# Optimization experiments

Measured on AMD Instinct MI355X. Metric: run time of the kernel, lower is better.

## Reference

```python
import jax, jax.numpy as jnp
import numpy as np

B, L, D, H = 8, 2048, 1024, 1024
BASE_LR, BASE_WD = 0.01, 0.9


def setup_inputs() -> dict:
    key = jax.random.key(0)
    ks = jax.random.split(key, 8)
    s = 1.0 / np.sqrt(D)
    return {
        "x": jax.random.normal(ks[0], (B, L, D), jnp.float32),
        "hidden": jax.random.normal(ks[1], (B, D, H), jnp.float32),
        "log_base_lr": jnp.array([np.log(BASE_LR)], jnp.float32),
        "w_lr": jax.random.normal(ks[2], (D, 1), jnp.float32) * s,
        "b_lr": jnp.zeros((1,), jnp.float32),
        "log_base_wd": jnp.array([np.log(BASE_WD)], jnp.float32),
        "w_wd": jax.random.normal(ks[3], (D, 1), jnp.float32) * s,
        "b_wd": jnp.zeros((1,), jnp.float32),
        "w_q": jax.random.normal(ks[4], (D, H), jnp.float32) * s,
        "b_q": jnp.zeros((H,), jnp.float32),
        "w_k": jax.random.normal(ks[5], (D, H), jnp.float32) * s,
        "b_k": jnp.zeros((H,), jnp.float32),
        "w_v": jax.random.normal(ks[6], (D, D), jnp.float32) * s,
        "b_v": jnp.zeros((D,), jnp.float32),
    }


def reference(x, hidden, log_base_lr, w_lr, b_lr, log_base_wd, w_wd, b_wd,
              w_q, b_q, w_k, b_k, w_v, b_v):
    batch, length, dim = x.shape
    W_prev = hidden  # [b, d, h]
    query = x @ w_q + b_q                     # [b, l, h]
    key = x @ w_k + b_k                       # [b, l, h]
    value = x @ w_v + b_v                     # [b, l, d]
    lr = jnp.exp(log_base_lr) * jax.nn.sigmoid((x @ w_lr + b_lr)[..., 0])  # [b, l]
    # log(1 - base_wd * sigmoid(.)) via log1p for stability; same math.
    log_wd = jnp.log1p(-jnp.exp(log_base_wd) * jax.nn.sigmoid((x @ w_wd + b_wd)[..., 0]))  # [b, l]
    wd_cross = jnp.exp(jnp.cumsum(log_wd, axis=1))  # [b, l]
    # inner-chunk decay: entry [b, m, l] = exp(sum_{j=m+1..l} log_wd[b, j]) for l >= m
    tri = jnp.triu(jnp.broadcast_to(log_wd[:, None, :], (batch, length, length)), k=1)
    wd_inner = jnp.triu(jnp.exp(jnp.cumsum(tri, axis=2)))  # [b, l, l]
    kq = jnp.einsum('bld,bmd->blm', key, query)            # [b, l, m]
    mask_kq = kq * wd_inner
    WpK_V = jnp.einsum('bdh,blh->bld', W_prev, key) - value  # [b, l, d]
    y_inner = -jnp.einsum('bld,bl,blm->bmd', WpK_V, lr, mask_kq)
    y_cross = jnp.einsum('bdh,blh,bl->bld', W_prev, query, wd_cross)
    y = y_inner + y_cross
    W_next_inner = -jnp.einsum('bld,bl,blh->bdh', WpK_V, lr * wd_inner[:, :, -1], key)
    W_next_cross = W_prev * wd_cross[:, -1][:, None, None]
    W_next = W_next_inner + W_next_cross
    return y, W_next
```

## Files before the change

### kernel.cpp

```cpp
#include <hip/hip_runtime.h>
#include <stdint.h>

#define BB 8
#define LL 2048
#define DD 1024
#define HH 1024
#define BL (BB*LL)

typedef __attribute__((ext_vector_type(8))) short short8;
typedef __attribute__((ext_vector_type(4))) float f32x4;

__device__ __forceinline__ unsigned short f2bf(float f) {
  unsigned int x = __float_as_uint(f);
  unsigned int r = (x + 0x7fffu + ((x >> 16) & 1u)) >> 16;
  return (unsigned short)r;
}
__device__ __forceinline__ float bf2f(unsigned short u) {
  return __uint_as_float(((unsigned int)u) << 16);
}

__device__ __forceinline__ void stage16(const unsigned short* g, unsigned short* l) {
  __builtin_amdgcn_global_load_lds((const __attribute__((address_space(1))) void*)g,
                                   (__attribute__((address_space(3))) void*)l,
                                   16, 0, 0);
}

#define TM 128
#define TN 128
#define BK 64

struct __align__(16) Smem {
  unsigned short a[TM*BK];
  unsigned short b[TN*BK];
};

__device__ __forceinline__ void gemm_core(const unsigned short* __restrict__ A, int lda,
                                          const unsigned short* __restrict__ B, int ldb,
                                          int m0, int n0, int ktiles,
                                          Smem* sm, f32x4 acc[4][4]) {
  const int tid  = threadIdx.x;
  const int lane = tid & 63;
  const int wave = tid >> 6;
  const int mw = (wave >> 1) * 64;
  const int nw = (wave & 1) * 64;
  const int srow = lane >> 3;
  const int scol = (((lane & 7) ^ srow) * 8);
  const int fk = (lane >> 4) * 8;
  const int fr = lane & 15;
  const int fx = fr & 7;
  for (int kt = 0; kt < ktiles; ++kt) {
    const int k0 = kt * BK;
#pragma unroll
    for (int r = 0; r < 4; ++r) {
      const int chunk = wave * 4 + r;
      const int row = chunk * 8 + srow;
      stage16(A + (size_t)(m0 + row) * lda + (k0 + scol), &sm->a[chunk * 512]);
      stage16(B + (size_t)(n0 + row) * ldb + (k0 + scol), &sm->b[chunk * 512]);
    }
    __syncthreads();
#pragma unroll
    for (int kk = 0; kk < BK; kk += 32) {
      const int kc = ((((kk + fk) >> 3) ^ fx) << 3);
      short8 af[4], bfv[4];
#pragma unroll
      for (int i = 0; i < 4; ++i)
        af[i] = *(const short8*)&sm->a[(mw + i*16 + fr) * BK + kc];
#pragma unroll
      for (int j = 0; j < 4; ++j)
        bfv[j] = *(const short8*)&sm->b[(nw + j*16 + fr) * BK + kc];
#pragma unroll
      for (int i = 0; i < 4; ++i)
#pragma unroll
        for (int j = 0; j < 4; ++j)
          acc[i][j] = __builtin_amdgcn_mfma_f32_16x16x32_bf16(af[i], bfv[j], acc[i][j], 0, 0, 0);
    }
    __syncthreads();
  }
}

__device__ __forceinline__ void acc_init(f32x4 acc[4][4]) {
#pragma unroll
  for (int i = 0; i < 4; ++i)
#pragma unroll
    for (int j = 0; j < 4; ++j)
      acc[i][j] = (f32x4){0.f, 0.f, 0.f, 0.f};
}

template <typename F>
__device__ __forceinline__ void epilogue_loop(const f32x4 acc[4][4], F body) {
  const int lane_ = threadIdx.x & 63;
  const int wave_ = threadIdx.x >> 6;
  const int mw_ = (wave_ >> 1) * 64, nw_ = (wave_ & 1) * 64;
#pragma unroll
  for (int mi = 0; mi < 4; ++mi)
#pragma unroll
    for (int ni = 0; ni < 4; ++ni)
#pragma unroll
      for (int j = 0; j < 4; ++j) {
        const int rr = mw_ + mi * 16 + ((lane_ >> 4) << 2) + j;
        const int cc = nw_ + ni * 16 + (lane_ & 15);
        body(rr, cc, acc[mi][ni][j]);
      }
}

template<int MI>
struct __align__(16) Smem2 {
  unsigned short a[2][MI*2048];
  unsigned short b[2][16384];
};

template<int MI>
__device__ __forceinline__ void acc_init2(f32x4 (&acc)[MI][4]) {
#pragma unroll
  for (int i = 0; i < MI; ++i)
#pragma unroll
    for (int j = 0; j < 4; ++j)
      acc[i][j] = (f32x4){0.f, 0.f, 0.f, 0.f};
}

template<int MI, class FA, class FB>
__device__ __forceinline__ void gemm2_core(FA srcA, FB srcB, int NK,
                                           Smem2<MI>* sm, f32x4 (&acc)[MI][4]) {
  const int lane = threadIdx.x & 63;
  const int wave = threadIdx.x >> 6;
  const int srow = lane >> 3;
  const int scol = ((lane & 7) ^ srow) * 8;
  constexpr int APW = MI / 2;
  const int fk = (lane >> 4) * 8;
  const int fr = lane & 15;
  const int fx = fr & 7;
  const int mwr = (wave >> 2) * (MI * 16);
  const int nwr = (wave & 3) * 64;

  auto STAGE = [&](int p, int kt) {
#pragma unroll
    for (int r = 0; r < APW; ++r) {
      const int chunk = wave * APW + r;
      stage16(srcA(chunk * 8 + srow, kt) + scol, &sm->a[p][chunk * 512]);
    }
#pragma unroll
    for (int r = 0; r < 4; ++r) {
      const int chunk = wave * 4 + r;
      stage16(srcB(chunk * 8 + srow, kt) + scol, &sm->b[p][chunk * 512]);
    }
  };
  auto COMPUTE = [&](int p) {
    const unsigned short* pa  = sm->a[p];
    const unsigned short* pbp = sm->b[p];
#pragma unroll
    for (int kk = 0; kk < 64; kk += 32) {
      const int kc = ((((kk + fk) >> 3) ^ fx) << 3);
      short8 af[MI], bfv[4];
#pragma unroll
      for (int i = 0; i < MI; ++i)
        af[i] = *(const short8*)&pa[(mwr + i*16 + fr) * 64 + kc];
#pragma unroll
      for (int j = 0; j < 4; ++j)
        bfv[j] = *(const short8*)&pbp[(nwr + j*16 + fr) * 64 + kc];
#pragma unroll
      for (int i = 0; i < MI; ++i)
#pragma unroll
        for (int j = 0; j < 4; ++j)
          acc[i][j] = __builtin_amdgcn_mfma_f32_16x16x32_bf16(af[i], bfv[j], acc[i][j], 0, 0, 0);
    }
  };

  STAGE(0, 0);
  asm volatile("s_waitcnt vmcnt(0)" ::: "memory");
  __builtin_amdgcn_s_barrier();
  __builtin_amdgcn_sched_barrier(0);
  int cur = 0;
  for (int kt = 0; kt < NK - 1; ++kt) {
    STAGE(cur ^ 1, kt + 1);
    COMPUTE(cur);
    asm volatile("s_waitcnt vmcnt(0)" ::: "memory");
    __builtin_amdgcn_s_barrier();
    __builtin_amdgcn_sched_barrier(0);
    cur ^= 1;
  }
  COMPUTE(cur);
}

template<int MI, typename F>
__device__ __forceinline__ void epi2(const f32x4 (&acc)[MI][4], F body) {
  const int lane = threadIdx.x & 63;
  const int wave = threadIdx.x >> 6;
  const int mwr = (wave >> 2) * (MI * 16), nwr = (wave & 3) * 64;
#pragma unroll
  for (int i = 0; i < MI; ++i)
#pragma unroll
    for (int j = 0; j < 4; ++j)
#pragma unroll
      for (int jj = 0; jj < 4; ++jj) {
        const int rr = mwr + i * 16 + ((lane >> 4) << 2) + jj;
        const int cc = nwr + j * 16 + (lane & 15);
        body(rr, cc, acc[i][j][jj]);
      }
}


__global__ void k_prep_x(const float* __restrict__ x, const float* __restrict__ wlr,
                         const float* __restrict__ wwd, unsigned short* __restrict__ xb,
                         float* __restrict__ lrlog, float* __restrict__ wdlog) {
  const int wave = threadIdx.x >> 6, lane = threadIdx.x & 63;
  const int row = blockIdx.x * 4 + wave;
  const float* xr = x + (size_t)row * DD;
  float s1 = 0.f, s2 = 0.f;
#pragma unroll
  for (int ch = 0; ch < 4; ++ch) {
    const int col = ch * 256 + lane * 4;
    float4 v = *(const float4*)(xr + col);
    float4 a = *(const float4*)(wlr + col);
    float4 b = *(const float4*)(wwd + col);
    s1 += v.x*a.x + v.y*a.y + v.z*a.z + v.w*a.w;
    s2 += v.x*b.x + v.y*b.y + v.z*b.z + v.w*b.w;
    uint2 u;
    u.x = (unsigned)f2bf(v.x) | ((unsigned)f2bf(v.y) << 16);
    u.y = (unsigned)f2bf(v.z) | ((unsigned)f2bf(v.w) << 16);
    *(uint2*)(xb + (size_t)row * DD + col) = u;
  }
#pragma unroll
  for (int off = 32; off > 0; off >>= 1) {
    s1 += __shfl_down(s1, off);
    s2 += __shfl_down(s2, off);
  }
  if (lane == 0) { lrlog[row] = s1; wdlog[row] = s2; }
}

__global__ void k_prep_w(const float* __restrict__ wq, const float* __restrict__ wk,
                         const float* __restrict__ wv, unsigned short* __restrict__ wqt,
                         unsigned short* __restrict__ wkt, unsigned short* __restrict__ wvtn,
                         unsigned short* __restrict__ wkr) {
  const int idx = blockIdx.x * 256 + threadIdx.x;
  if (blockIdx.z == 3) { wkr[idx] = f2bf(wk[idx]); return; }
  const int k = idx >> 10, n = idx & 1023;
  const float* src = (blockIdx.z == 0) ? wq : (blockIdx.z == 1) ? wk : wv;
  unsigned short* dst = (blockIdx.z == 0) ? wqt : (blockIdx.z == 1) ? wkt : wvtn;
  float v = src[(size_t)k * 1024 + n];
  if (blockIdx.z == 2) v = -v;
  dst[(size_t)n * 1024 + k] = f2bf(v);
}

__global__ void k_prep_h(const float* __restrict__ hid, unsigned short* __restrict__ wpb) {
  const size_t i = ((size_t)blockIdx.x * 256 + threadIdx.x) * 4;
  float4 v = *(const float4*)(hid + i);
  uint2 u;
  u.x = (unsigned)f2bf(v.x) | ((unsigned)f2bf(v.y) << 16);
  u.y = (unsigned)f2bf(v.z) | ((unsigned)f2bf(v.w) << 16);
  *(uint2*)(wpb + i) = u;
}

__global__ void k_bias2(const unsigned short* __restrict__ wpb, const float* __restrict__ bk,
                        const float* __restrict__ bv, float* __restrict__ bias2) {
  const int wave = threadIdx.x >> 6, lane = threadIdx.x & 63;
  const int row = blockIdx.x * 4 + wave;
  const unsigned short* wr = wpb + (size_t)row * HH;
  float s = 0.f;
#pragma unroll
  for (int ch = 0; ch < 4; ++ch) {
    const int col = ch * 256 + lane * 4;
    float4 a = *(const float4*)(bk + col);
    ushort4 u = *(const ushort4*)(wr + col);
    s += a.x * bf2f(u.x) + a.y * bf2f(u.y) + a.z * bf2f(u.z) + a.w * bf2f(u.w);
  }
#pragma unroll
  for (int off = 32; off > 0; off >>= 1) s += __shfl_down(s, off);
  if (lane == 0) bias2[row] = s - bv[row & 1023];
}

__global__ void k_scan(const float* __restrict__ lrlog, const float* __restrict__ wdlog,
                       const float* __restrict__ lbl, const float* __restrict__ blr,
                       const float* __restrict__ lbw, const float* __restrict__ bwd,
                       float* __restrict__ lr, float* __restrict__ c,
                       float* __restrict__ s, float* __restrict__ ecl) {
  const int b = blockIdx.x, t = threadIdx.x;
  __shared__ float sums[256];
  const float elr = expf(lbl[0]);
  const float ewd = expf(lbw[0]);
  const float blr0 = blr[0], bwd0 = bwd[0];
  float lw[8];
  const float* wb = wdlog + (size_t)b * LL + t * 8;
  float tot = 0.f;
#pragma unroll
  for (int i = 0; i < 8; ++i) {
    float z = wb[i] + bwd0;
    float sig = 1.f / (1.f + expf(-z));
    tot += log1pf(-ewd * sig);
    lw[i] = tot;
  }
  sums[t] = tot;
  __syncthreads();
  for (int off = 1; off < 256; off <<= 1) {
    float v = (t >= off) ? sums[t - off] : 0.f;
    __syncthreads();
    sums[t] += v;
    __syncthreads();
  }
  const float prev = (t > 0) ? sums[t - 1] : 0.f;
  const float ctot = sums[255];
  const float* lb = lrlog + (size_t)b * LL + t * 8;
#pragma unroll
  for (int i = 0; i < 8; ++i) {
    const int idx = b * LL + t * 8 + i;
    const float ci = prev + lw[i];
    c[idx] = ci;
    float zl = lb[i] + blr0;
    float lri = elr / (1.f + expf(-zl));
    lr[idx] = lri;
    s[idx] = lri * expf(ctot - ci);
  }
  if (t == 0) ecl[b] = expf(ctot);
}


__global__ __launch_bounds__(512, 2) void k2_gemm_m2(const unsigned short* __restrict__ wpb,
    const unsigned short* __restrict__ wkr, const unsigned short* __restrict__ wvtn,
    unsigned short* __restrict__ w2t) {
  __shared__ Smem2<4> sm;
  const int b = blockIdx.x;
  const int mt = blockIdx.y & 7, nt = blockIdx.y >> 3;
  const int m0 = mt * 128, n0 = nt * 256;
  f32x4 acc[4][4]; acc_init2<4>(acc);
  gemm2_core<4>(
    [&](int r, int kt) { return wpb + (size_t)b * DD * HH + (size_t)(m0 + r) * HH + kt * 64; },
    [&](int r, int kt) { return wkr + (size_t)(n0 + r) * HH + kt * 64; },
    HH / 64, &sm, acc);
  epi2<4>(acc, [&](int rr, int cc, float av) {
    const size_t gi = (size_t)(m0 + rr) * DD + (n0 + cc);
    w2t[(size_t)b * DD * DD + gi] = f2bf(av + bf2f(wvtn[gi]));
  });
}

__global__ __launch_bounds__(512, 2) void k2_gemm_q(const unsigned short* __restrict__ xb,
    const unsigned short* __restrict__ wt, const float* __restrict__ bias,
    const float* __restrict__ c, unsigned short* __restrict__ outb,
    unsigned short* __restrict__ q2b) {
  __shared__ Smem2<8> sm;
  const int mt = blockIdx.x * 8 + (blockIdx.y & 7);
  const int nt = blockIdx.y >> 3;
  const int m0 = mt * 256, n0 = nt * 256;
  f32x4 acc[8][4]; acc_init2<8>(acc);
  gemm2_core<8>(
    [&](int r, int kt) { return xb + (size_t)(m0 + r) * DD + kt * 64; },
    [&](int r, int kt) { return wt + (size_t)(n0 + r) * DD + kt * 64; },
    DD / 64, &sm, acc);
  epi2<8>(acc, [&](int rr, int cc, float av) {
    const int row = m0 + rr, col = n0 + cc;
    const float v = av + bias[col];
    outb[(size_t)row * HH + col] = f2bf(v);
    q2b[(size_t)row * HH + col] = f2bf(v * __expf(c[row]));
  });
}

__global__ __launch_bounds__(512, 2) void k2_gemm_k(const unsigned short* __restrict__ xb,
    const unsigned short* __restrict__ wt, const float* __restrict__ bias,
    const float* __restrict__ s, unsigned short* __restrict__ kb,
    unsigned short* __restrict__ k2t) {
  __shared__ Smem2<8> sm;
  const int mt = blockIdx.x * 8 + (blockIdx.y & 7);
  const int nt = blockIdx.y >> 3;
  const int m0 = mt * 256, n0 = nt * 256;
  f32x4 acc[8][4]; acc_init2<8>(acc);
  gemm2_core<8>(
    [&](int r, int kt) { return xb + (size_t)(m0 + r) * DD + kt * 64; },
    [&](int r, int kt) { return wt + (size_t)(n0 + r) * DD + kt * 64; },
    DD / 64, &sm, acc);
  const int lane = threadIdx.x & 63, wave = threadIdx.x >> 6;
  const int mwr = (wave >> 2) * 128, nwr = (wave & 3) * 64;
#pragma unroll
  for (int i = 0; i < 8; ++i)
#pragma unroll
    for (int j = 0; j < 4; ++j) {
      const int col = n0 + nwr + j*16 + (lane & 15);
      const float bias_c = bias[col];
      const int row0 = m0 + mwr + i*16 + ((lane >> 4) << 2);
      const int b = row0 >> 11, ml0 = row0 & 2047;
      unsigned short tmp[4];
#pragma unroll
      for (int jj = 0; jj < 4; ++jj) {
        float v = acc[i][j][jj] + bias_c;
        kb[(size_t)(row0 + jj) * HH + col] = f2bf(v);
        tmp[jj] = f2bf(v * s[row0 + jj]);
      }
      uint2 u;
      u.x = (unsigned)tmp[0] | ((unsigned)tmp[1] << 16);
      u.y = (unsigned)tmp[2] | ((unsigned)tmp[3] << 16);
      *(uint2*)&k2t[((size_t)b * HH + col) * LL + ml0] = u;
    }
}

__global__ __launch_bounds__(512, 2) void k2_gemm_u(const unsigned short* __restrict__ xb,
    const unsigned short* __restrict__ w2t, const float* __restrict__ bias2,
    unsigned short* __restrict__ ut) {
  __shared__ Smem2<8> sm;
  const int b = blockIdx.x;
  const int mt = blockIdx.x * 8 + (blockIdx.y & 7);
  const int nt = blockIdx.y >> 3;
  const int m0 = mt * 256, n0 = nt * 256;
  f32x4 acc[8][4]; acc_init2<8>(acc);
  gemm2_core<8>(
    [&](int r, int kt) { return xb + (size_t)(m0 + r) * DD + kt * 64; },
    [&](int r, int kt) { return w2t + (size_t)b * DD * DD + (size_t)(n0 + r) * DD + kt * 64; },
    DD / 64, &sm, acc);
  const int lane = threadIdx.x & 63, wave = threadIdx.x >> 6;
  const int mwr = (wave >> 2) * 128, nwr = (wave & 3) * 64;
#pragma unroll
  for (int i = 0; i < 8; ++i)
#pragma unroll
    for (int j = 0; j < 4; ++j) {
      const int col = n0 + nwr + j*16 + (lane & 15);
      const float b2c = bias2[b * DD + col];
      const int row0 = m0 + mwr + i*16 + ((lane >> 4) << 2);
      const int ml0 = row0 & 2047;
      unsigned short tmp[4];
#pragma unroll
      for (int jj = 0; jj < 4; ++jj) tmp[jj] = f2bf(acc[i][j][jj] + b2c);
      uint2 u;
      u.x = (unsigned)tmp[0] | ((unsigned)tmp[1] << 16);
      u.y = (unsigned)tmp[2] | ((unsigned)tmp[3] << 16);
      *(uint2*)&ut[((size_t)b * DD + col) * LL + ml0] = u;
    }
}

__global__ __launch_bounds__(256) void k_gemm_p(const unsigned short* __restrict__ qb,
    const unsigned short* __restrict__ kb, const float* __restrict__ lr,
    const float* __restrict__ c, unsigned short* __restrict__ pb) {
  const int b = blockIdx.z;
  const int i = blockIdx.x;
  const int t = (i & 7) * 17 + (i >> 3);
  int mt = (int)((sqrtf(8.0f * (float)t + 1.0f) - 1.0f) * 0.5f);
  while ((mt + 1) * (mt + 2) / 2 <= t) ++mt;
  while (mt * (mt + 1) / 2 > t) --mt;
  const int nt = t - mt * (mt + 1) / 2;
  __shared__ Smem sm;
  f32x4 acc[4][4]; acc_init(acc);
  const int base = b * LL;
  const int m0g = base + mt * TM, n0g = base + nt * TN;
  gemm_core(qb, HH, kb, HH, m0g, n0g, HH / BK, &sm, acc);

  const int lane = threadIdx.x & 63, wave = threadIdx.x >> 6;
  const int mw = (wave >> 1) * 64, nw = (wave & 1) * 64;
  if (nt != mt) {
    const float cref = c[base + mt * TM];
    float er[4][4], fc[4];
#pragma unroll
    for (int mi = 0; mi < 4; ++mi)
#pragma unroll
      for (int j = 0; j < 4; ++j) {
        const int m = mt * TM + mw + mi*16 + ((lane >> 4) << 2) + j;
        er[mi][j] = __expf(c[base + m] - cref);
      }
#pragma unroll
    for (int ni = 0; ni < 4; ++ni) {
      const int l = nt * TN + nw + ni*16 + (lane & 15);
      fc[ni] = lr[base + l] * __expf(cref - c[base + l]);
    }
#pragma unroll
    for (int mi = 0; mi < 4; ++mi)
#pragma unroll
      for (int ni = 0; ni < 4; ++ni) {
        const int l = nt * TN + nw + ni*16 + (lane & 15);
        const int row0 = mt * TM + mw + mi*16 + ((lane >> 4) << 2);
#pragma unroll
        for (int j = 0; j < 4; ++j) {
          const float v = -acc[mi][ni][j] * er[mi][j] * fc[ni];
          pb[((size_t)base + row0 + j) * LL + l] = f2bf(v);
        }
      }
  } else {
    epilogue_loop(acc, [&](int rr, int cc, float av) {
      const int m = mt * TM + rr, l = nt * TN + cc;
      float v = 0.f;
      if (l <= m) v = -av * lr[base + l] * __expf(c[base + m] - c[base + l]);
      pb[((size_t)base + m) * LL + l] = f2bf(v);
    });
  }
}

__global__ __launch_bounds__(512, 2) void k2_gemm_y(const unsigned short* __restrict__ pb,
    const unsigned short* __restrict__ ut, const unsigned short* __restrict__ q2b,
    const unsigned short* __restrict__ wpb, float* __restrict__ out) {
  __shared__ Smem2<4> sm;
  const int b = blockIdx.x;
  const int mt = 15 - (blockIdx.y & 15);
  const int nt = blockIdx.y >> 4;
  const int m0 = mt * 128, n0 = nt * 256;
  const int NK1 = (mt + 1) * 2;
  f32x4 acc[4][4]; acc_init2<4>(acc);
  gemm2_core<4>(
    [&](int r, int kt) {
      return (kt < NK1) ? pb + (size_t)b * LL * LL + (size_t)(m0 + r) * LL + kt * 64
                        : q2b + ((size_t)b * LL + m0 + r) * HH + (kt - NK1) * 64;
    },
    [&](int r, int kt) {
      return (kt < NK1) ? ut + (size_t)b * DD * LL + (size_t)(n0 + r) * LL + kt * 64
                        : wpb + (size_t)b * DD * HH + (size_t)(n0 + r) * HH + (kt - NK1) * 64;
    },
    NK1 + 16, &sm, acc);
  epi2<4>(acc, [&](int rr, int cc, float av) {
    out[((size_t)b * LL + m0 + rr) * DD + (n0 + cc)] = av;
  });
}

__global__ __launch_bounds__(512, 2) void k2_gemm_wn(const unsigned short* __restrict__ ut,
    const unsigned short* __restrict__ k2t, const float* __restrict__ hid,
    const float* __restrict__ ecl, float* __restrict__ out2) {
  __shared__ Smem2<4> sm;
  const int b = blockIdx.x;
  const int mt = blockIdx.y & 7, nt = blockIdx.y >> 3;
  const int m0 = mt * 128, n0 = nt * 256;
  f32x4 acc[4][4]; acc_init2<4>(acc);
  gemm2_core<4>(
    [&](int r, int kt) { return ut + (size_t)b * DD * LL + (size_t)(m0 + r) * LL + kt * 64; },
    [&](int r, int kt) { return k2t + (size_t)b * HH * LL + (size_t)(n0 + r) * LL + kt * 64; },
    LL / 64, &sm, acc);
  const float eclb = ecl[b];
  epi2<4>(acc, [&](int rr, int cc, float av) {
    const size_t gi = ((size_t)b * DD + (m0 + rr)) * HH + (n0 + cc);
    out2[gi] = -av + eclb * hid[gi];
  });
}


extern "C" void kernel_launch(void* const* d_in, const int* in_sizes, int n_in,
                              void* d_out, int out_size, void* d_ws, size_t ws_size,
                              hipStream_t stream) {
  (void)in_sizes; (void)n_in; (void)out_size; (void)ws_size;
  const float* x   = (const float*)d_in[0];
  const float* hid = (const float*)d_in[1];
  const float* lbl = (const float*)d_in[2];
  const float* wlr = (const float*)d_in[3];
  const float* blr = (const float*)d_in[4];
  const float* lbw = (const float*)d_in[5];
  const float* wwd = (const float*)d_in[6];
  const float* bwd = (const float*)d_in[7];
  const float* wq  = (const float*)d_in[8];
  const float* bq  = (const float*)d_in[9];
  const float* wk  = (const float*)d_in[10];
  const float* bk  = (const float*)d_in[11];
  const float* wv  = (const float*)d_in[12];
  const float* bv  = (const float*)d_in[13];
  float* out = (float*)d_out;

  char* w = (char*)d_ws;
  constexpr size_t SZ_XB  = (size_t)BL * DD * 2;
  constexpr size_t SZ_QB  = (size_t)BL * HH * 2;
  constexpr size_t SZ_KB  = (size_t)BL * HH * 2;
  constexpr size_t SZ_K2T = (size_t)BB * HH * LL * 2;
  constexpr size_t SZ_UT  = (size_t)BB * DD * LL * 2;
  constexpr size_t SZ_PB  = (size_t)BB * LL * LL * 2;
  constexpr size_t SZ_WT  = (size_t)DD * HH * 2;
  constexpr size_t SZ_WPB = (size_t)BB * DD * HH * 2;
  constexpr size_t SZ_V16 = (size_t)BL * 4;

  size_t off = 0;
  unsigned short* xb   = (unsigned short*)(w + off); off += SZ_XB;
  unsigned short* qb   = (unsigned short*)(w + off); off += SZ_QB;
  unsigned short* kb   = (unsigned short*)(w + off); off += SZ_KB;
  unsigned short* k2t  = (unsigned short*)(w + off); off += SZ_K2T;
  unsigned short* ut   = (unsigned short*)(w + off); off += SZ_UT;
  unsigned short* pb   = (unsigned short*)(w + off); off += SZ_PB;
  unsigned short* wqt  = (unsigned short*)(w + off); off += SZ_WT;
  unsigned short* wkt  = (unsigned short*)(w + off); off += SZ_WT;
  unsigned short* wvtn = (unsigned short*)(w + off); off += SZ_WT;
  unsigned short* wpb  = (unsigned short*)(w + off); off += SZ_WPB;
  float* lrlog = (float*)(w + off); off += SZ_V16;
  float* wdlog = (float*)(w + off); off += SZ_V16;
  float* lr    = (float*)(w + off); off += SZ_V16;
  float* c     = (float*)(w + off); off += SZ_V16;
  float* s     = (float*)(w + off); off += SZ_V16;
  float* ecl   = (float*)(w + off); off += 256;
  float* bias2 = (float*)(w + off); off += (size_t)BB * DD * 4;

  unsigned short* w2t = pb;
  unsigned short* wkr = pb + (size_t)BB * DD * DD;

  unsigned short* q2b = (unsigned short*)(out + (size_t)BL * DD);
  float* out2 = out + (size_t)BL * DD;

  k_prep_x<<<dim3(BL / 4), 256, 0, stream>>>(x, wlr, wwd, xb, lrlog, wdlog);
  k_prep_w<<<dim3(4096, 1, 4), 256, 0, stream>>>(wq, wk, wv, wqt, wkt, wvtn, wkr);
  k_prep_h<<<dim3((unsigned)((size_t)BB * DD * HH / 1024)), 256, 0, stream>>>(hid, wpb);
  k_scan<<<dim3(BB), 256, 0, stream>>>(lrlog, wdlog, lbl, blr, lbw, bwd, lr, c, s, ecl);
  k_bias2<<<dim3(BB * DD / 4), 256, 0, stream>>>(wpb, bk, bv, bias2);

  k2_gemm_m2<<<dim3(8, 32), 512, 0, stream>>>(wpb, wkr, wvtn, w2t);
  k2_gemm_q<<<dim3(8, 32), 512, 0, stream>>>(xb, wqt, bq, c, qb, q2b);
  k2_gemm_k<<<dim3(8, 32), 512, 0, stream>>>(xb, wkt, bk, s, kb, k2t);
  k2_gemm_u<<<dim3(8, 32), 512, 0, stream>>>(xb, w2t, bias2, ut);
  k_gemm_p<<<dim3(136, 1, BB), 256, 0, stream>>>(qb, kb, lr, c, pb);
  k2_gemm_y<<<dim3(8, 64), 512, 0, stream>>>(pb, ut, q2b, wpb, out);
  k2_gemm_wn<<<dim3(8, 32), 512, 0, stream>>>(ut, k2t, hid, ecl, out2);
}
```

Before: 628.4 us.

## Generalize GEMM pipeline to configurable prefetch depth and retile causal P GEMM

Replaces the double-buffered GEMM core with a ring-buffered core whose prefetch depth is a template parameter. It waits on partial vmcnt counts so several K-tiles of loads can be in flight while compute proceeds. The 4-wide-M kernels now use a triple buffer (depth 2), while the 8-wide-M kernels keep depth 1. The causal QK^T kernel moves from a 256-thread 128x128 tile core to the shared 512-thread 128x256 pipelined core, with a new lower-triangular tile mapping. That mapping computes some wasted upper-triangle work and uses more LDS per block, which can limit occupancy.

```diff
diff --git a/kernel.cpp b/kernel.cpp
--- a/kernel.cpp
+++ b/kernel.cpp
@@ -25,107 +25,38 @@
                                    16, 0, 0);
 }
 
-#define TM 128
-#define TN 128
-#define BK 64
-
-struct __align__(16) Smem {
-  unsigned short a[TM*BK];
-  unsigned short b[TN*BK];
+template<int N> struct WaitVm;
+#define WVM(N) template<> struct WaitVm<N> { \
+  static __device__ __forceinline__ void w() { \
+    asm volatile("s_waitcnt vmcnt(" #N ")" ::: "memory"); } };
+WVM(0) WVM(6) WVM(8) WVM(12)
+#undef WVM
+
+template<int MI, int PD>
+struct __align__(16) Smem3 {
+  unsigned short a[PD+1][MI*2048];
+  unsigned short b[PD+1][16384];
 };
 
-__device__ __forceinline__ void gemm_core(const unsigned short* __restrict__ A, int lda,
-                                          const unsigned short* __restrict__ B, int ldb,
-                                          int m0, int n0, int ktiles,
-                                          Smem* sm, f32x4 acc[4][4]) {
-  const int tid  = threadIdx.x;
-  const int lane = tid & 63;
-  const int wave = tid >> 6;
-  const int mw = (wave >> 1) * 64;
-  const int nw = (wave & 1) * 64;
-  const int srow = lane >> 3;
-  const int scol = (((lane & 7) ^ srow) * 8);
-  const int fk = (lane >> 4) * 8;
-  const int fr = lane & 15;
-  const int fx = fr & 7;
-  for (int kt = 0; kt < ktiles; ++kt) {
-    const int k0 = kt * BK;
-#pragma unroll
-    for (int r = 0; r < 4; ++r) {
-      const int chunk = wave * 4 + r;
-      const int row = chunk * 8 + srow;
-      stage16(A + (size_t)(m0 + row) * lda + (k0 + scol), &sm->a[chunk * 512]);
-      stage16(B + (size_t)(n0 + row) * ldb + (k0 + scol), &sm->b[chunk * 512]);
-    }
-    __syncthreads();
-#pragma unroll
-    for (int kk = 0; kk < BK; kk += 32) {
-      const int kc = ((((kk + fk) >> 3) ^ fx) << 3);
-      short8 af[4], bfv[4];
-#pragma unroll
-      for (int i = 0; i < 4; ++i)
-        af[i] = *(const short8*)&sm->a[(mw + i*16 + fr) * BK + kc];
-#pragma unroll
-      for (int j = 0; j < 4; ++j)
-        bfv[j] = *(const short8*)&sm->b[(nw + j*16 + fr) * BK + kc];
-#pragma unroll
-      for (int i = 0; i < 4; ++i)
-#pragma unroll
-        for (int j = 0; j < 4; ++j)
-          acc[i][j] = __builtin_amdgcn_mfma_f32_16x16x32_bf16(af[i], bfv[j], acc[i][j], 0, 0, 0);
-    }
-    __syncthreads();
-  }
-}
-
-__device__ __forceinline__ void acc_init(f32x4 acc[4][4]) {
-#pragma unroll
-  for (int i = 0; i < 4; ++i)
+template<int MI>
+__device__ __forceinline__ void acc_init2(f32x4 (&acc)[MI][4]) {
+#pragma unroll
+  for (int i = 0; i < MI; ++i)
 #pragma unroll
     for (int j = 0; j < 4; ++j)
       acc[i][j] = (f32x4){0.f, 0.f, 0.f, 0.f};
 }
 
-template <typename F>
-__device__ __forceinline__ void epilogue_loop(const f32x4 acc[4][4], F body) {
-  const int lane_ = threadIdx.x & 63;
-  const int wave_ = threadIdx.x >> 6;
-  const int mw_ = (wave_ >> 1) * 64, nw_ = (wave_ & 1) * 64;
-#pragma unroll
-  for (int mi = 0; mi < 4; ++mi)
-#pragma unroll
-    for (int ni = 0; ni < 4; ++ni)
-#pragma unroll
-      for (int j = 0; j < 4; ++j) {
-        const int rr = mw_ + mi * 16 + ((lane_ >> 4) << 2) + j;
-        const int cc = nw_ + ni * 16 + (lane_ & 15);
-        body(rr, cc, acc[mi][ni][j]);
-      }
-}
-
-template<int MI>
-struct __align__(16) Smem2 {
-  unsigned short a[2][MI*2048];
-  unsigned short b[2][16384];
-};
-
-template<int MI>
-__device__ __forceinline__ void acc_init2(f32x4 (&acc)[MI][4]) {
-#pragma unroll
-  for (int i = 0; i < MI; ++i)
-#pragma unroll
-    for (int j = 0; j < 4; ++j)
-      acc[i][j] = (f32x4){0.f, 0.f, 0.f, 0.f};
-}
-
-template<int MI, class FA, class FB>
-__device__ __forceinline__ void gemm2_core(FA srcA, FB srcB, int NK,
-                                           Smem2<MI>* sm, f32x4 (&acc)[MI][4]) {
+template<int MI, int PD, class FA, class FB>
+__device__ __forceinline__ void gemm3_core(FA srcA, FB srcB, int NK,
+                                           Smem3<MI,PD>* sm, f32x4 (&acc)[MI][4]) {
+  constexpr int NB  = PD + 1;
+  constexpr int APW = MI / 2;
+  constexpr int LPW = APW + 4;
   const int lane = threadIdx.x & 63;
   const int wave = threadIdx.x >> 6;
   const int srow = lane >> 3;
   const int scol = ((lane & 7) ^ srow) * 8;
-  constexpr int APW = MI / 2;
   const int fk = (lane >> 4) * 8;
   const int fr = lane & 15;
   const int fx = fr & 7;
@@ -165,20 +96,26 @@
     }
   };
 
-  STAGE(0, 0);
-  asm volatile("s_waitcnt vmcnt(0)" ::: "memory");
-  __builtin_amdgcn_s_barrier();
-  __builtin_amdgcn_sched_barrier(0);
-  int cur = 0;
-  for (int kt = 0; kt < NK - 1; ++kt) {
-    STAGE(cur ^ 1, kt + 1);
-    COMPUTE(cur);
-    asm volatile("s_waitcnt vmcnt(0)" ::: "memory");
+#pragma unroll
+  for (int d = 0; d < PD; ++d) STAGE(d, d);
+  int pc = 0;
+  int ps = PD % NB;
+  for (int kt = 0; kt < NK; ++kt) {
+    if (kt + PD < NK) {
+      STAGE(ps, kt + PD);
+      ps = (ps + 1 == NB) ? 0 : ps + 1;
+      WaitVm<PD * LPW>::w();
+    } else if (PD == 2 && kt + PD == NK) {
+      WaitVm<LPW>::w();
+    } else {
+      WaitVm<0>::w();
+    }
     __builtin_amdgcn_s_barrier();
     __builtin_amdgcn_sched_barrier(0);
-    cur ^= 1;
-  }
-  COMPUTE(cur);
+    COMPUTE(pc);
+    pc = (pc + 1 == NB) ? 0 : pc + 1;
+    __builtin_amdgcn_s_barrier();
+  }
 }
 
 template<int MI, typename F>
@@ -313,15 +250,15 @@
 }
 
 
-__global__ __launch_bounds__(512, 2) void k2_gemm_m2(const unsigned short* __restrict__ wpb,
+__global__ __launch_bounds__(512, 2) void k3_gemm_m2(const unsigned short* __restrict__ wpb,
     const unsigned short* __restrict__ wkr, const unsigned short* __restrict__ wvtn,
     unsigned short* __restrict__ w2t) {
-  __shared__ Smem2<4> sm;
+  __shared__ Smem3<4,2> sm;
   const int b = blockIdx.x;
   const int mt = blockIdx.y & 7, nt = blockIdx.y >> 3;
   const int m0 = mt * 128, n0 = nt * 256;
   f32x4 acc[4][4]; acc_init2<4>(acc);
-  gemm2_core<4>(
+  gemm3_core<4,2>(
     [&](int r, int kt) { return wpb + (size_t)b * DD * HH + (size_t)(m0 + r) * HH + kt * 64; },
     [&](int r, int kt) { return wkr + (size_t)(n0 + r) * HH + kt * 64; },
     HH / 64, &sm, acc);
@@ -331,16 +268,16 @@
   });
 }
 
-__global__ __launch_bounds__(512, 2) void k2_gemm_q(const unsigned short* __restrict__ xb,
+__global__ __launch_bounds__(512, 2) void k3_gemm_q(const unsigned short* __restrict__ xb,
     const unsigned short* __restrict__ wt, const float* __restrict__ bias,
     const float* __restrict__ c, unsigned short* __restrict__ outb,
     unsigned short* __restrict__ q2b) {
-  __shared__ Smem2<8> sm;
+  __shared__ Smem3<8,1> sm;
   const int mt = blockIdx.x * 8 + (blockIdx.y & 7);
   const int nt = blockIdx.y >> 3;
   const int m0 = mt * 256, n0 = nt * 256;
   f32x4 acc[8][4]; acc_init2<8>(acc);
-  gemm2_core<8>(
+  gemm3_core<8,1>(
     [&](int r, int kt) { return xb + (size_t)(m0 + r) * DD + kt * 64; },
     [&](int r, int kt) { return wt + (size_t)(n0 + r) * DD + kt * 64; },
     DD / 64, &sm, acc);
@@ -352,16 +289,16 @@
   });
 }
 
-__global__ __launch_bounds__(512, 2) void k2_gemm_k(const unsigned short* __restrict__ xb,
+__global__ __launch_bounds__(512, 2) void k3_gemm_k(const unsigned short* __restrict__ xb,
     const unsigned short* __restrict__ wt, const float* __restrict__ bias,
     const float* __restrict__ s, unsigned short* __restrict__ kb,
     unsigned short* __restrict__ k2t) {
-  __shared__ Smem2<8> sm;
+  __shared__ Smem3<8,1> sm;
   const int mt = blockIdx.x * 8 + (blockIdx.y & 7);
   const int nt = blockIdx.y >> 3;
   const int m0 = mt * 256, n0 = nt * 256;
   f32x4 acc[8][4]; acc_init2<8>(acc);
-  gemm2_core<8>(
+  gemm3_core<8,1>(
     [&](int r, int kt) { return xb + (size_t)(m0 + r) * DD + kt * 64; },
     [&](int r, int kt) { return wt + (size_t)(n0 + r) * DD + kt * 64; },
     DD / 64, &sm, acc);
@@ -389,16 +326,16 @@
     }
 }
 
-__global__ __launch_bounds__(512, 2) void k2_gemm_u(const unsigned short* __restrict__ xb,
+__global__ __launch_bounds__(512, 2) void k3_gemm_u(const unsigned short* __restrict__ xb,
     const unsigned short* __restrict__ w2t, const float* __restrict__ bias2,
     unsigned short* __restrict__ ut) {
-  __shared__ Smem2<8> sm;
+  __shared__ Smem3<8,1> sm;
   const int b = blockIdx.x;
   const int mt = blockIdx.x * 8 + (blockIdx.y & 7);
   const int nt = blockIdx.y >> 3;
   const int m0 = mt * 256, n0 = nt * 256;
   f32x4 acc[8][4]; acc_init2<8>(acc);
-  gemm2_core<8>(
+  gemm3_core<8,1>(
     [&](int r, int kt) { return xb + (size_t)(m0 + r) * DD + kt * 64; },
     [&](int r, int kt) { return w2t + (size_t)b * DD * DD + (size_t)(n0 + r) * DD + kt * 64; },
     DD / 64, &sm, acc);
@@ -422,72 +359,44 @@
     }
 }
 
-__global__ __launch_bounds__(256) void k_gemm_p(const unsigned short* __restrict__ qb,
+__global__ __launch_bounds__(512, 2) void k3_gemm_p(const unsigned short* __restrict__ qb,
     const unsigned short* __restrict__ kb, const float* __restrict__ lr,
     const float* __restrict__ c, unsigned short* __restrict__ pb) {
-  const int b = blockIdx.z;
-  const int i = blockIdx.x;
-  const int t = (i & 7) * 17 + (i >> 3);
-  int mt = (int)((sqrtf(8.0f * (float)t + 1.0f) - 1.0f) * 0.5f);
-  while ((mt + 1) * (mt + 2) / 2 <= t) ++mt;
-  while (mt * (mt + 1) / 2 > t) --mt;
-  const int nt = t - mt * (mt + 1) / 2;
-  __shared__ Smem sm;
-  f32x4 acc[4][4]; acc_init(acc);
+  __shared__ Smem3<4,2> sm;
+  const int b = blockIdx.x;
+  const int t = blockIdx.y;
+  int r = (int)((sqrtf(4.f * (float)t + 1.f) - 1.f) * 0.5f);
+  while ((r + 1) * (r + 2) <= t) ++r;
+  while (r * (r + 1) > t) --r;
+  const int u = t - r * (r + 1);
+  const int mt = 2 * r + (u > r ? 1 : 0);
+  const int nt2 = (u > r) ? (u - r - 1) : u;
   const int base = b * LL;
-  const int m0g = base + mt * TM, n0g = base + nt * TN;
-  gemm_core(qb, HH, kb, HH, m0g, n0g, HH / BK, &sm, acc);
-
-  const int lane = threadIdx.x & 63, wave = threadIdx.x >> 6;
-  const int mw = (wave >> 1) * 64, nw = (wave & 1) * 64;
-  if (nt != mt) {
-    const float cref = c[base + mt * TM];
-    float er[4][4], fc[4];
-#pragma unroll
-    for (int mi = 0; mi < 4; ++mi)
-#pragma unroll
-      for (int j = 0; j < 4; ++j) {
-        const int m = mt * TM + mw + mi*16 + ((lane >> 4) << 2) + j;
-        er[mi][j] = __expf(c[base + m] - cref);
-      }
-#pragma unroll
-    for (int ni = 0; ni < 4; ++ni) {
-      const int l = nt * TN + nw + ni*16 + (lane & 15);
-      fc[ni] = lr[base + l] * __expf(cref - c[base + l]);
-    }
-#pragma unroll
-    for (int mi = 0; mi < 4; ++mi)
-#pragma unroll
-      for (int ni = 0; ni < 4; ++ni) {
-        const int l = nt * TN + nw + ni*16 + (lane & 15);
-        const int row0 = mt * TM + mw + mi*16 + ((lane >> 4) << 2);
-#pragma unroll
-        for (int j = 0; j < 4; ++j) {
-          const float v = -acc[mi][ni][j] * er[mi][j] * fc[ni];
-          pb[((size_t)base + row0 + j) * LL + l] = f2bf(v);
-        }
-      }
-  } else {
-    epilogue_loop(acc, [&](int rr, int cc, float av) {
-      const int m = mt * TM + rr, l = nt * TN + cc;
-      float v = 0.f;
-      if (l <= m) v = -av * lr[base + l] * __expf(c[base + m] - c[base + l]);
-      pb[((size_t)base + m) * LL + l] = f2bf(v);
-    });
-  }
-}
-
-__global__ __launch_bounds__(512, 2) void k2_gemm_y(const unsigned short* __restrict__ pb,
+  const int m0 = mt * 128, n0 = nt2 * 256;
+  f32x4 acc[4][4]; acc_init2<4>(acc);
+  gemm3_core<4,2>(
+    [&](int rr, int kt) { return qb + (size_t)(base + m0 + rr) * HH + kt * 64; },
+    [&](int rr, int kt) { return kb + (size_t)(base + n0 + rr) * HH + kt * 64; },
+    HH / 64, &sm, acc);
+  epi2<4>(acc, [&](int rr, int cc, float av) {
+    const int m = m0 + rr, l = n0 + cc;
+    float v = 0.f;
+    if (l <= m) v = -av * lr[base + l] * __expf(c[base + m] - c[base + l]);
+    pb[((size_t)base + m) * LL + l] = f2bf(v);
+  });
+}
+
+__global__ __launch_bounds__(512, 2) void k3_gemm_y(const unsigned short* __restrict__ pb,
     const unsigned short* __restrict__ ut, const unsigned short* __restrict__ q2b,
     const unsigned short* __restrict__ wpb, float* __restrict__ out) {
-  __shared__ Smem2<4> sm;
+  __shared__ Smem3<4,2> sm;
   const int b = blockIdx.x;
   const int mt = 15 - (blockIdx.y & 15);
   const int nt = blockIdx.y >> 4;
   const int m0 = mt * 128, n0 = nt * 256;
   const int NK1 = (mt + 1) * 2;
   f32x4 acc[4][4]; acc_init2<4>(acc);
-  gemm2_core<4>(
+  gemm3_core<4,2>(
     [&](int r, int kt) {
       return (kt < NK1) ? pb + (size_t)b * LL * LL + (size_t)(m0 + r) * LL + kt * 64
                         : q2b + ((size_t)b * LL + m0 + r) * HH + (kt - NK1) * 64;
@@ -502,15 +411,15 @@
   });
 }
 
-__global__ __launch_bounds__(512, 2) void k2_gemm_wn(const unsigned short* __restrict__ ut,
+__global__ __launch_bounds__(512, 2) void k3_gemm_wn(const unsigned short* __restrict__ ut,
     const unsigned short* __restrict__ k2t, const float* __restrict__ hid,
     const float* __restrict__ ecl, float* __restrict__ out2) {
-  __shared__ Smem2<4> sm;
+  __shared__ Smem3<4,2> sm;
   const int b = blockIdx.x;
   const int mt = blockIdx.y & 7, nt = blockIdx.y >> 3;
   const int m0 = mt * 128, n0 = nt * 256;
   f32x4 acc[4][4]; acc_init2<4>(acc);
-  gemm2_core<4>(
+  gemm3_core<4,2>(
     [&](int r, int kt) { return ut + (size_t)b * DD * LL + (size_t)(m0 + r) * LL + kt * 64; },
     [&](int r, int kt) { return k2t + (size_t)b * HH * LL + (size_t)(n0 + r) * LL + kt * 64; },
     LL / 64, &sm, acc);
@@ -584,11 +493,11 @@
   k_scan<<<dim3(BB), 256, 0, stream>>>(lrlog, wdlog, lbl, blr, lbw, bwd, lr, c, s, ecl);
   k_bias2<<<dim3(BB * DD / 4), 256, 0, stream>>>(wpb, bk, bv, bias2);
 
-  k2_gemm_m2<<<dim3(8, 32), 512, 0, stream>>>(wpb, wkr, wvtn, w2t);
-  k2_gemm_q<<<dim3(8, 32), 512, 0, stream>>>(xb, wqt, bq, c, qb, q2b);
-  k2_gemm_k<<<dim3(8, 32), 512, 0, stream>>>(xb, wkt, bk, s, kb, k2t);
-  k2_gemm_u<<<dim3(8, 32), 512, 0, stream>>>(xb, w2t, bias2, ut);
-  k_gemm_p<<<dim3(136, 1, BB), 256, 0, stream>>>(qb, kb, lr, c, pb);
-  k2_gemm_y<<<dim3(8, 64), 512, 0, stream>>>(pb, ut, q2b, wpb, out);
-  k2_gemm_wn<<<dim3(8, 32), 512, 0, stream>>>(ut, k2t, hid, ecl, out2);
-}
+  k3_gemm_m2<<<dim3(8, 32), 512, 0, stream>>>(wpb, wkr, wvtn, w2t);
+  k3_gemm_q<<<dim3(8, 32), 512, 0, stream>>>(xb, wqt, bq, c, qb, q2b);
+  k3_gemm_k<<<dim3(8, 32), 512, 0, stream>>>(xb, wkt, bk, s, kb, k2t);
+  k3_gemm_u<<<dim3(8, 32), 512, 0, stream>>>(xb, w2t, bias2, ut);
+  k3_gemm_p<<<dim3(8, 72), 512, 0, stream>>>(qb, kb, lr, c, pb);
+  k3_gemm_y<<<dim3(8, 64), 512, 0, stream>>>(pb, ut, q2b, wpb, out);
+  k3_gemm_wn<<<dim3(8, 32), 512, 0, stream>>>(ut, k2t, hid, ecl, out2);
+}
```

Result: faster. 615.9 us (-2.0%).
